# Kernel tuning notes

Hardware: AMD Instinct MI355X
Metric: run time of the kernel (lower is better)

The kernel has to match this reference:

```python
import jax, jax.numpy as jnp
import numpy as np

N_NODES = 2048
N_EDGES = 65536
IN_CH, HID_CH, OUT_CH = 512, 256, 128
NDIM = 5
THRESHOLD = 0.5


def _gcn(x, src, dst, ew, W, b):
    # GCNConv with self-loops (weight 1): D^{-1/2}(A+I)D^{-1/2} X W + b
    n = x.shape[0]
    deg = jnp.zeros((n,), x.dtype).at[dst].add(ew) + 1.0
    dinv = 1.0 / jnp.sqrt(deg)
    h = x @ W  # [N, out]
    coef = ew * dinv[src] * dinv[dst]  # [E]
    agg = jnp.zeros_like(h).at[dst].add(h[src] * coef[:, None])
    return agg + h / deg[:, None] + b


def _class_flags(feat, thr):
    # cosine similarity -> unnormalized Laplacian -> eigengap-based class ids
    xn = feat / (jnp.linalg.norm(feat, axis=1, keepdims=True) + 1e-8)
    S = xn @ xn.T  # [N, N]
    L = jnp.diag(jnp.sum(S, axis=1)) - S
    vals = jnp.linalg.eigvalsh(jax.lax.stop_gradient(L))  # ascending (class ids are non-diff)
    gaps = jnp.diff(vals)
    return jnp.concatenate([jnp.zeros((1,), jnp.int32),
                            jnp.cumsum((gaps > thr).astype(jnp.int32))])


def _class_avg(flags, feat):
    # per-class mean features, gathered back to each node
    n = feat.shape[0]
    sums = jax.ops.segment_sum(feat, flags, num_segments=n)
    cnts = jax.ops.segment_sum(jnp.ones((n,), feat.dtype), flags, num_segments=n)
    avg = sums / jnp.maximum(cnts, 1.0)[:, None]
    return avg[flags]


def _block(prev_gcn, skip, srcs, dsts, ews, convW, convb, linW, linb, k,
           changeW=None, changeb=None):
    gcn_out, outs = [], []
    for i in range(NDIM):
        g = _gcn(prev_gcn[i], srcs[i], dsts[i], ews[i], convW[i], convb[i])
        flags = _class_flags(g, THRESHOLD)
        lin = _class_avg(flags, g) @ linW + linb
        fir = skip[i] @ changeW + changeb if changeW is not None else skip[i]
        fea = fir + k * lin  # add_class_avg_to_node_features
        outs.append(jax.nn.relu(fir + fea))
        gcn_out.append(g)
    return gcn_out, outs


def _forward(dims, edge_indices, edge_weights, convWs, convbs, linWs, linbs,
             change1_W, change1_b, change2_W, change2_b, dimension_weights, k_save):
    srcs = [edge_indices[i, 0] for i in range(NDIM)]
    dsts = [edge_indices[i, 1] for i in range(NDIM)]
    ews = [edge_weights[i] for i in range(NDIM)]
    w = dimension_weights / jnp.sum(dimension_weights)
    g, out = _block(dims, dims, srcs, dsts, ews, convWs[0], convbs[0], linWs[0], linbs[0], k_save, change1_W, change1_b)
    g, out = _block(g, out, srcs, dsts, ews, convWs[1], convbs[1], linWs[1], linbs[1], k_save, change2_W, change2_b)
    for layer in range(2, 6):
        g, out = _block(g, out, srcs, dsts, ews, convWs[layer], convbs[layer], linWs[layer], linbs[layer], k_save)
    # dimension-weighted fusion of final per-dimension outputs
    return sum(w[i] * out[i] for i in range(NDIM))


def setup_inputs() -> dict:
    key = jax.random.key(0)
    ks = iter(jax.random.split(key, 80))
    def nrm(shape, s=0.05):
        return (jax.random.normal(next(ks), shape, jnp.float32) * s)
    inp = {}
    for i in range(NDIM):
        inp[f"dim{i+1}"] = jax.random.normal(next(ks), (N_NODES, IN_CH), jnp.float32)
    inp["edge_indices"] = jax.random.randint(next(ks), (NDIM, 2, N_EDGES), 0, N_NODES, jnp.int32)
    inp["edge_weights"] = jax.random.uniform(next(ks), (NDIM, N_EDGES), jnp.float32)
    inp["non_zero"] = N_NODES
    conv_shapes = [(IN_CH, HID_CH), (HID_CH, OUT_CH)] + [(OUT_CH, OUT_CH)] * 4
    for l, (ci, co) in enumerate(conv_shapes, start=1):
        inp[f"convW{l}"] = nrm((NDIM, ci, co))
        inp[f"convb{l}"] = nrm((NDIM, co))
    lin_shapes = [HID_CH, OUT_CH, OUT_CH, OUT_CH, OUT_CH, OUT_CH]
    names = ["preLin1", "preLin2", "preLin3", "behLin1", "behLin2", "behLin3"]
    for nm, c in zip(names, lin_shapes):
        inp[f"{nm}_W"] = nrm((c, c))
        inp[f"{nm}_b"] = nrm((c,))
    inp["change1_W"] = nrm((IN_CH, HID_CH)); inp["change1_b"] = nrm((HID_CH,))
    inp["change2_W"] = nrm((HID_CH, OUT_CH)); inp["change2_b"] = nrm((OUT_CH,))
    inp["dimension_weights"] = jnp.ones((NDIM,), jnp.float32)
    inp["k_save"] = jnp.float32(0.5)
    return inp


def reference(dim1, dim2, dim3, dim4, dim5, edge_indices, edge_weights, non_zero,
              convW1, convb1, convW2, convb2, convW3, convb3, convW4, convb4,
              convW5, convb5, convW6, convb6,
              preLin1_W, preLin1_b, preLin2_W, preLin2_b, preLin3_W, preLin3_b,
              behLin1_W, behLin1_b, behLin2_W, behLin2_b, behLin3_W, behLin3_b,
              change1_W, change1_b, change2_W, change2_b, dimension_weights, k_save):
    dims = [dim1, dim2, dim3, dim4, dim5]
    convWs = [convW1, convW2, convW3, convW4, convW5, convW6]
    convbs = [convb1, convb2, convb3, convb4, convb5, convb6]
    linWs = [preLin1_W, preLin2_W, preLin3_W, behLin1_W, behLin2_W, behLin3_W]
    linbs = [preLin1_b, preLin2_b, preLin3_b, behLin1_b, behLin2_b, behLin3_b]
    return _forward(dims, edge_indices, edge_weights, convWs, convbs, linWs, linbs,
                    change1_W, change1_b, change2_W, change2_b, dimension_weights, k_save)
```

## Files before the change

### kernel.cpp

```cpp
#include <hip/hip_runtime.h>
#include <math.h>
#include <stdint.h>

#define NN 2048
#define NE 65536
#define ND 5
#define DMX 256
#define MAXB1 2048
#define SUBD 8
#define NBF (MAXB1*SUBD+1)
#define NFMAX 1536
#define MAXRUN 1536
#define NPB 4
#define COARSE_H 1.76f
#define NUDGE 2e-3f
#define THRG 0.5f

typedef float f32x16 __attribute__((ext_vector_type(16)));
typedef float f32x8 __attribute__((ext_vector_type(8)));
typedef short s16x8 __attribute__((ext_vector_type(8)));
typedef unsigned short u16x8 __attribute__((ext_vector_type(8)));

__device__ __forceinline__ float wredSum(float v){
#pragma unroll
  for (int o=32;o>0;o>>=1) v += __shfl_down(v,o,64);
  return v;
}
__device__ __forceinline__ float wredMin(float v){
#pragma unroll
  for (int o=32;o>0;o>>=1) v = fminf(v,__shfl_down(v,o,64));
  return v;
}
__device__ __forceinline__ float wredMax(float v){
#pragma unroll
  for (int o=32;o>0;o>>=1) v = fmaxf(v,__shfl_down(v,o,64));
  return v;
}
__device__ __forceinline__ uint32_t encF(float f){
  uint32_t u = __float_as_uint(f);
  return (u & 0x80000000u) ? ~u : (u | 0x80000000u);
}
__device__ __forceinline__ float decF(uint32_t u){
  return (u & 0x80000000u) ? __uint_as_float(u ^ 0x80000000u) : __uint_as_float(~u);
}
__device__ __forceinline__ uint16_t bf16hi(float f){
  return (uint16_t)(__float_as_uint(f)>>16);
}

template<int BLK>
__device__ float bredSum(float v, float* red){
  v = wredSum(v);
  const int w = threadIdx.x >> 6;
  if ((threadIdx.x & 63) == 0) red[w] = v;
  __syncthreads();
  if (threadIdx.x == 0){
    float s = 0.f;
#pragma unroll
    for (int i=0;i<BLK/64;i++) s += red[i];
    red[0] = s;
  }
  __syncthreads();
  float r = red[0];
  __syncthreads();
  return r;
}

__global__ void k_prep(const float* __restrict__ xn, uint16_t* __restrict__ xph,
                       uint16_t* __restrict__ xpl, float* __restrict__ xpf, int co){
  const int dim = blockIdx.y;
  const int c2 = blockIdx.x;
  const int col = threadIdx.x;
  const float* x = xn + (size_t)dim*NN*co;
  const int kb = c2*8;
  u16x8 h8, l8;
  f32x8 f8;
#pragma unroll
  for (int j=0;j<8;j++){
    const float x0 = x[(size_t)(kb+j)*co + col];
    const uint16_t h = bf16hi(x0);
    h8[j] = h;
    l8[j] = bf16hi(x0 - __uint_as_float((uint32_t)h<<16));
    f8[j] = x0;
  }
  const size_t o = ((size_t)dim*(NN/8) + c2)*co + col;
  reinterpret_cast<u16x8*>(xph)[o] = h8;
  reinterpret_cast<u16x8*>(xpl)[o] = l8;
  reinterpret_cast<f32x8*>(xpf)[o] = f8;
}

template<int D, int BLK>
__device__ int evalNu(const uint16_t* __restrict__ xph, const uint16_t* __restrict__ xpl,
                      const float* __restrict__ xpf,
                      const float* __restrict__ a,
                      float t0, float dlt,
                      float* M, float* Pt, float* red, float* wrow,
                      float* scal, float* tOut)
{
  const int tid = threadIdx.x;
  float* fsc = scal + 16;

  float md = 1e30f;
  for (int i=tid;i<NN;i+=BLK) md = fminf(md, fabsf(a[i]-t0));
  md = wredMin(md);
  if ((tid & 63) == 0) red[tid>>6] = md;
  __syncthreads();
  if (tid == 0){
    float m2 = 1e30f;
    for (int i=0;i<BLK/64;i++) m2 = fminf(m2, red[i]);
    scal[1] = (m2 < 1e-3f) ? (t0 + dlt) : t0;
  }
  __syncthreads();
  const float t = scal[1];
  __syncthreads();

  float c = 0.f;
  for (int i=tid;i<NN;i+=BLK) c += (a[i] < t) ? 1.f : 0.f;
  float cnt = bredSum<BLK>(c, red);

  constexpr int BG  = D/64;
  constexpr int NBL = BG*(BG+1)/2;
  constexpr int SXT = 24;
  static_assert(BLK == NBL*64, "one wave per tile block");
  static_assert(2*D*SXT*2 <= (D*(D+1)/2)*4, "WX overlay fits in M");

  uint16_t* WXh = reinterpret_cast<uint16_t*>(M);
  uint16_t* WXl = WXh + D*SXT;
  const f32x8* XPF = reinterpret_cast<const f32x8*>(xpf);

  const int wv_ = tid >> 6, lane = tid & 63;
  int bi = 0, bj = 0;
  { int rem = wv_; while (rem >= BG - bi){ rem -= BG - bi; bi++; } bj = bi + rem; }
  const int colA = bi*64 + (lane & 31);
  const int colB = bj*64 + (lane & 31);
  const int kgo  = (lane >> 5) * 8;

  f32x16 acc0, acc1, acc2, acc3;
#pragma unroll
  for (int e=0;e<16;e++){ acc0[e]=0.f; acc1[e]=0.f; acc2[e]=0.f; acc3[e]=0.f; }

  if (tid < 16){
    float den = a[tid] - t;
    if (fabsf(den) < 1e-5f) den = (den < 0.f) ? -1e-5f : 1e-5f;
    wrow[tid] = 1.0f/den;
  }

  for (int k0=0; k0<NN; k0+=16){
    __syncthreads();
    const float* wcur = wrow + ((k0>>4)&1)*16;
    for (int it = tid; it < 2*D; it += BLK){
      const int kg  = it / D;
      const int col = it - kg*D;
      const f32x8 xv = XPF[(size_t)((k0>>3)+kg)*D + col];
      const float4 w0 = *reinterpret_cast<const float4*>(&wcur[kg*8]);
      const float4 w1 = *reinterpret_cast<const float4*>(&wcur[kg*8+4]);
      const float wv[8] = {w0.x,w0.y,w0.z,w0.w,w1.x,w1.y,w1.z,w1.w};
      u16x8 sph, spl;
#pragma unroll
      for (int j=0;j<8;j++){
        const float p0 = wv[j]*xv[j];
        const uint16_t hp = bf16hi(p0);
        sph[j] = hp;
        spl[j] = bf16hi(p0 - __uint_as_float((uint32_t)hp<<16));
      }
      const int base = col*SXT + kg*8;
      *reinterpret_cast<u16x8*>(WXh + base) = sph;
      *reinterpret_cast<u16x8*>(WXl + base) = spl;
    }
    if (tid < 16 && k0+16 < NN){
      float den = a[k0+16+tid] - t;
      if (fabsf(den) < 1e-5f) den = (den < 0.f) ? -1e-5f : 1e-5f;
      wrow[((((k0>>4)+1)&1)<<4) + tid] = 1.0f/den;
    }
    __syncthreads();
    const s16x8 ah0 = *reinterpret_cast<const s16x8*>(WXh + colA*SXT + kgo);
    const s16x8 ah1 = *reinterpret_cast<const s16x8*>(WXh + (colA+32)*SXT + kgo);
    const s16x8 al0 = *reinterpret_cast<const s16x8*>(WXl + colA*SXT + kgo);
    const s16x8 al1 = *reinterpret_cast<const s16x8*>(WXl + (colA+32)*SXT + kgo);
    const size_t cgB = (size_t)((k0>>3) + (lane>>5))*D;
    const s16x8 bh0 = *reinterpret_cast<const s16x8*>(xph + (cgB + colB)*8);
    const s16x8 bh1 = *reinterpret_cast<const s16x8*>(xph + (cgB + colB+32)*8);
    const s16x8 bl0 = *reinterpret_cast<const s16x8*>(xpl + (cgB + colB)*8);
    const s16x8 bl1 = *reinterpret_cast<const s16x8*>(xpl + (cgB + colB+32)*8);
    acc0 = __builtin_amdgcn_mfma_f32_32x32x16_bf16(ah0, bh0, acc0, 0,0,0);
    acc1 = __builtin_amdgcn_mfma_f32_32x32x16_bf16(ah0, bh1, acc1, 0,0,0);
    acc2 = __builtin_amdgcn_mfma_f32_32x32x16_bf16(ah1, bh0, acc2, 0,0,0);
    acc3 = __builtin_amdgcn_mfma_f32_32x32x16_bf16(ah1, bh1, acc3, 0,0,0);
    acc0 = __builtin_amdgcn_mfma_f32_32x32x16_bf16(ah0, bl0, acc0, 0,0,0);
    acc1 = __builtin_amdgcn_mfma_f32_32x32x16_bf16(ah0, bl1, acc1, 0,0,0);
    acc2 = __builtin_amdgcn_mfma_f32_32x32x16_bf16(ah1, bl0, acc2, 0,0,0);
    acc3 = __builtin_amdgcn_mfma_f32_32x32x16_bf16(ah1, bl1, acc3, 0,0,0);
    acc0 = __builtin_amdgcn_mfma_f32_32x32x16_bf16(al0, bh0, acc0, 0,0,0);
    acc1 = __builtin_amdgcn_mfma_f32_32x32x16_bf16(al0, bh1, acc1, 0,0,0);
    acc2 = __builtin_amdgcn_mfma_f32_32x32x16_bf16(al1, bh0, acc2, 0,0,0);
    acc3 = __builtin_amdgcn_mfma_f32_32x32x16_bf16(al1, bh1, acc3, 0,0,0);
  }
  __syncthreads();

  {
    const int rbase = 4*(lane>>5);
#pragma unroll
    for (int q=0;q<4;q++){
      const f32x16 A = (q==0)?acc0:((q==1)?acc1:((q==2)?acc2:acc3));
      const int ta = 2*bi + (q>>1), tb = 2*bj + (q&1);
      const int bb = tb*32 + (lane & 31);
#pragma unroll
      for (int r=0;r<16;r++){
        const int aa = ta*32 + (r&3) + 8*(r>>2) + rbase;
        if (aa <= bb)
          M[aa*D - (aa*(aa-1))/2 + (bb-aa)] = ((aa==bb)?1.f:0.f) - A[r];
      }
    }
  }

  constexpr int PS = 12;
  int neg = 0;
  for (int k0=0; k0<D; k0+=8){
    const int k1 = k0+8;
    __syncthreads();
    if (tid < 64){
      if (tid == 0){
        float B[8][8];
#pragma unroll
        for (int q=0;q<8;q++){
#pragma unroll
          for (int p=0;p<=q;p++){
            const int g = k0+p;
            B[p][q] = M[g*D - (g*(g-1))/2 + (k0+q-g)];
          }
        }
        float inv8[8];
#pragma unroll
        for (int q=0;q<8;q++){
          float d = B[q][q];
          if (d < 0.f) neg++;
          if (fabsf(d) < 1e-8f) d = (d<0.f)?-1e-8f:1e-8f;
          const float inv = 1.0f/d;
          inv8[q] = inv;
#pragma unroll
          for (int i=q+1;i<8;i++){
            const float f = B[q][i]*inv;
#pragma unroll
            for (int j=i;j<8;j++) B[i][j] = fmaf(-f, B[q][j], B[i][j]);
          }
        }
#pragma unroll
        for (int q=0;q<8;q++){
          fsc[36+q] = inv8[q];
#pragma unroll
          for (int p=0;p<=q;p++) fsc[(q*(q+1))/2 + p] = B[p][q];
        }
      }
      __asm__ __volatile__("s_waitcnt lgkmcnt(0)" ::: "memory");
      float c8[36], iv8[8];
#pragma unroll
      for (int k=0;k<36;k++) c8[k] = fsc[k];
#pragma unroll
      for (int k=0;k<8;k++) iv8[k] = fsc[36+k];
      for (int j = k1 + tid; j < D; j += 64){
        float rv[8], pt[8];
#pragma unroll
        for (int q=0;q<8;q++){
          const int g = k0+q;
          rv[q] = M[g*D - (g*(g-1))/2 + (j-g)];
        }
#pragma unroll
        for (int q=0;q<8;q++){
          float v = rv[q];
#pragma unroll
          for (int p=0;p<q;p++) v = fmaf(-c8[(q*(q+1))/2 + p], pt[p], v);
          pt[q] = v * iv8[q];
          const int g = k0+q;
          M[g*D - (g*(g-1))/2 + (j-g)] = v;
          Pt[j*PS + q] = pt[q];
        }
      }
    }
    __syncthreads();
    if (k1 < D){
      constexpr int G = BLK/4;
      const int grp = tid / G, sub = tid % G;
      for (int i0=k1; i0<D; i0+=4){
        const int i = i0 + grp;
        float cq[8];
#pragma unroll
        for (int q=0;q<8;q++){
          const int g = k0+q;
          cq[q] = M[g*D - (g*(g-1))/2 + (i-g)];
        }
        const int offi = i*D - (i*(i-1))/2;
        for (int j=i+sub; j<D; j+=G){
          const float4 p0 = *reinterpret_cast<const float4*>(&Pt[j*PS + 0]);
          const float4 p1 = *reinterpret_cast<const float4*>(&Pt[j*PS + 4]);
          float v = M[offi + (j-i)];
          v = fmaf(-cq[0],p0.x,v); v = fmaf(-cq[1],p0.y,v);
          v = fmaf(-cq[2],p0.z,v); v = fmaf(-cq[3],p0.w,v);
          v = fmaf(-cq[4],p1.x,v); v = fmaf(-cq[5],p1.y,v);
          v = fmaf(-cq[6],p1.z,v); v = fmaf(-cq[7],p1.w,v);
          M[offi + (j-i)] = v;
        }
      }
    }
  }
  if (tid == 0) ((int*)scal)[5] = neg;
  __syncthreads();
  const int negAll = ((int*)scal)[5];
  __syncthreads();

  *tOut = t;
  return negAll + (int)(cnt + 0.5f);
}

#define SMEM_D(D) (((D)*((D)+1)/2 + 12*(D) + 112)*4)

template<int D, int BLK, int WPE>
__global__ __launch_bounds__(BLK,WPE) void k_eval(const uint16_t* __restrict__ xph,
    const uint16_t* __restrict__ xpl, const float* __restrict__ xpf,
    const float* __restrict__ ab, const float* __restrict__ ctrlF,
    const int* __restrict__ ctrlI, int* __restrict__ nu1, float* __restrict__ tus1)
{
  const int dim = blockIdx.y;
  const int b = blockIdx.x;
  if (b > ctrlI[dim*8+0]) return;
  extern __shared__ float smem[];
  constexpr int TRI = D*(D+1)/2;
  float* M = smem; float* Pt = M+TRI; float* red = Pt + 12*D;
  float* wrow = red+16; float* scal = wrow+32;
  const float lo = ctrlF[dim*8+0], h1 = ctrlF[dim*8+1];
  float tU;
  int v = evalNu<D,BLK>(xph + (size_t)dim*NN*D, xpl + (size_t)dim*NN*D,
                        xpf + (size_t)dim*NN*D,
                        ab + dim*NN, lo + h1*b, NUDGE,
                        M,Pt,red,wrow,scal,&tU);
  if (threadIdx.x == 0){ nu1[dim*(MAXB1+1)+b] = v; tus1[dim*(MAXB1+1)+b] = tU; }
}

template<int D, int BLK, int WPE>
__global__ __launch_bounds__(BLK,WPE) void k_evalF(const uint16_t* __restrict__ xph,
    const uint16_t* __restrict__ xpl, const float* __restrict__ xpf,
    const float* __restrict__ ab, const float* __restrict__ ctrlF,
    const int* __restrict__ ctrlI, const int* __restrict__ fineBins,
    int* __restrict__ nuF, float* __restrict__ tusF)
{
  const int dim = blockIdx.y;
  const int task = blockIdx.x / (SUBD-1);
  int cnt = ctrlI[dim*8+3]; if (cnt > NFMAX) cnt = NFMAX;
  if (task >= cnt) return;
  const int s = blockIdx.x % (SUBD-1) + 1;
  const int bin = fineBins[dim*NFMAX + task];
  extern __shared__ float smem[];
  constexpr int TRI = D*(D+1)/2;
  float* M = smem; float* Pt = M+TRI; float* red = Pt + 12*D;
  float* wrow = red+16; float* scal = wrow+32;
  const float lo = ctrlF[dim*8+0], hf = ctrlF[dim*8+1]*(1.0f/SUBD);
  const int f = bin*SUBD + s;
  float tU;
  int v = evalNu<D,BLK>(xph + (size_t)dim*NN*D, xpl + (size_t)dim*NN*D,
                        xpf + (size_t)dim*NN*D,
                        ab + dim*NN, lo + hf*f, NUDGE,
                        M,Pt,red,wrow,scal,&tU);
  if (threadIdx.x == 0){ nuF[(size_t)dim*NBF+f] = v; tusF[(size_t)dim*NBF+f] = tU; }
}

template<int D, int BLK, int WPE>
__global__ __launch_bounds__(BLK,WPE) void k_probe(const uint16_t* __restrict__ xph,
    const uint16_t* __restrict__ xpl, const float* __restrict__ xpf,
    const float* __restrict__ ab, const int* __restrict__ ctrlI,
    const int* __restrict__ runP, const float* __restrict__ runB,
    int* __restrict__ nuP, float* __restrict__ tP)
{
  const int dim = blockIdx.y;
  const int r = blockIdx.x >> 3;
  int nr = ctrlI[dim*8+1]; if (nr > MAXRUN) nr = MAXRUN;
  if (r >= nr) return;
  const int side = (blockIdx.x >> 2) & 1;
  const int i = blockIdx.x & 3;
  extern __shared__ float smem[];
  constexpr int TRI = D*(D+1)/2;
  float* M = smem; float* Pt = M+TRI; float* red = Pt + 12*D;
  float* wrow = red+16; float* scal = wrow+32;
  const float* rb = runB + (size_t)(dim*MAXRUN + r)*4;
  const float lo = rb[side*2+0], hi = rb[side*2+1];
  const float t0 = lo + (hi - lo)*(float)(i+1)*(1.0f/(NPB+1));
  const float dlt = fminf(NUDGE, (hi-lo)*0.08f);
  float tU;
  int v = evalNu<D,BLK>(xph + (size_t)dim*NN*D, xpl + (size_t)dim*NN*D,
                        xpf + (size_t)dim*NN*D,
                        ab + dim*NN, t0, dlt,
                        M,Pt,red,wrow,scal,&tU);
  if (threadIdx.x == 0){
    const size_t o = (((size_t)dim*MAXRUN + r)*2 + side)*NPB + i;
    nuP[o] = v; tP[o] = tU;
  }
}

__global__ void k_decide(const int* __restrict__ ctrlI, const int* __restrict__ runP,
                         const float* __restrict__ runB, const int* __restrict__ nuP,
                         const float* __restrict__ tP, int* __restrict__ bnd){
  const int dim = blockIdx.x;
  int nr = ctrlI[dim*8+1]; if (nr > MAXRUN) nr = MAXRUN;
  for (int r = threadIdx.x; r < nr; r += blockDim.x){
    const int p = runP[dim*MAXRUN + r];
    const float* rb = runB + (size_t)(dim*MAXRUN + r)*4;
    float lam[2];
    for (int side=0; side<2; side++){
      const int rank = p + side;
      const size_t o = (((size_t)dim*MAXRUN + r)*2 + side)*NPB;
      float prev = rb[side*2+0];
      bool found = false; float l = 0.f;
      for (int i=0;i<NPB;i++){
        const float ti = tP[o+i];
        if (nuP[o+i] >= rank){ l = 0.5f*(prev + ti); found = true; break; }
        prev = ti;
      }
      if (!found) l = 0.5f*(prev + rb[side*2+1]);
      lam[side] = l;
    }
    if (lam[1] - lam[0] > THRG) bnd[dim*NN + p - 1] = 1;
  }
}

__global__ void k_sel(const int* __restrict__ nu1, int* ctrlI,
                      int* __restrict__ binSel, int* __restrict__ fineBins){
  const int dim = blockIdx.y;
  const int j = blockIdx.x*256 + threadIdx.x;
  const int nb1 = ctrlI[dim*8+0];
  if (j >= nb1) return;
  const int* nv = nu1 + dim*(MAXB1+1);
  if (nv[j+1] != nv[j]){
    const int slot = atomicAdd(&ctrlI[dim*8+3], 1);
    if (slot < NFMAX){ binSel[dim*MAXB1+j] = slot; fineBins[dim*NFMAX+slot] = j; }
    else binSel[dim*MAXB1+j] = -2;
  } else binSel[dim*MAXB1+j] = -1;
}

__global__ void k_fill(const int* __restrict__ nu1, const float* __restrict__ tus1,
                       const int* __restrict__ binSel, const float* __restrict__ ctrlF,
                       const int* __restrict__ ctrlI,
                       int* __restrict__ nuF, float* __restrict__ tusF){
  const int dim = blockIdx.y;
  const int f = blockIdx.x*256 + threadIdx.x;
  const int nb1 = ctrlI[dim*8+0];
  if (f > nb1*SUBD) return;
  const int j = f / SUBD, s = f % SUBD;
  const float lo = ctrlF[dim*8+0], hf = ctrlF[dim*8+1]*(1.0f/SUBD);
  int v; float tv;
  if (s == 0){ v = nu1[dim*(MAXB1+1)+j]; tv = tus1[dim*(MAXB1+1)+j]; }
  else {
    const int sel = binSel[dim*MAXB1+j];
    tv = lo + hf*f;
    if (sel == -2) v = 0x40000000 + f;
    else v = nu1[dim*(MAXB1+1)+j];
  }
  nuF[(size_t)dim*NBF+f] = v;
  tusF[(size_t)dim*NBF+f] = tv;
}

__global__ void k_runs(const int* __restrict__ nuF, const float* __restrict__ tusF,
                       int* ctrlI, int* __restrict__ runP, float* __restrict__ runB,
                       int* __restrict__ bnd){
  const int dim = blockIdx.y;
  const int b1 = blockIdx.x*256 + threadIdx.x;
  const int nbt = ctrlI[dim*8+0]*SUBD;
  if (b1 >= nbt) return;
  const int* nv = nuF + (size_t)dim*NBF;
  const float* tu = tusF + (size_t)dim*NBF;
  if (nv[b1+1] != nv[b1]) return;
  if (b1 > 0 && nv[b1-1] == nv[b1]) return;
  const int p = nv[b1];
  if (p < 1 || p > NN-1 || b1 < 1) return;
  const float tb1 = tu[b1];
  int j2 = b1;
  while (j2+1 < nbt && nv[j2+2] == nv[j2+1]){
    j2++;
    if (tu[j2+1] - tb1 > THRG){ bnd[dim*NN + p-1] = 1; return; }
  }
  if (j2 > nbt-2) return;
  const float gmin = tu[j2+1] - tb1;
  const float gmax = tu[j2+2] - tu[b1-1];
  if (gmin > THRG){ bnd[dim*NN + p-1] = 1; return; }
  if (gmax > THRG){
    const int slot = atomicAdd(&ctrlI[dim*8+1], 1);
    if (slot < MAXRUN){
      runP[dim*MAXRUN + slot] = p;
      float* rb = runB + (size_t)(dim*MAXRUN + slot)*4;
      rb[0]=tu[b1-1]; rb[1]=tu[b1]; rb[2]=tu[j2+1]; rb[3]=tu[j2+2];
    }
  }
}

__global__ void k_pw_init(float* __restrict__ vG, float* __restrict__ scACC){
  const int dim = blockIdx.x, tid = threadIdx.x;
  float* v = vG + (size_t)dim*NN;
  for (int i=tid;i<NN;i+=1024){
    uint32_t hsh = (uint32_t)i*2654435761u;
    v[i] = 1.0f + 2e-4f*(float)(hsh>>20);
  }
  if (tid == 0){ scACC[0*ND*2 + dim*2 + 0] = 1.0f; scACC[0*ND*2 + dim*2 + 1] = 0.f; }
}

template<int D>
__global__ __launch_bounds__(D) void k_pw_z(const float* __restrict__ xnb,
    const float* __restrict__ vG, float* __restrict__ zpart,
    float* __restrict__ scACC, int parReset){
  const int dim = blockIdx.y, seg = blockIdx.x, c = threadIdx.x;
  const float* x = xnb + (size_t)dim*NN*D;
  const float* v = vG + (size_t)dim*NN;
  const int i0 = seg*(NN/16);
  float acc = 0.f;
  for (int r=0;r<NN/16;r++){
    const int i = i0 + r;
    acc = fmaf(x[(size_t)i*D + c], v[i], acc);
  }
  zpart[((size_t)dim*16 + seg)*DMX + c] = acc;
  if (seg == 0 && c < 2) scACC[parReset*ND*2 + dim*2 + c] = 0.f;
}

template<int D>
__global__ __launch_bounds__(256) void k_pw_y(const float* __restrict__ xnb,
    const float* __restrict__ ab, const uint32_t* __restrict__ ctrlU,
    const float* __restrict__ zpart, float* __restrict__ vG,
    float* __restrict__ scACC, int parPrev, int parCur){
  constexpr int VEC = D/64;
  const int dim = blockIdx.y, seg = blockIdx.x, tid = threadIdx.x;
  const int w = tid >> 6, lane = tid & 63;
  const float* x = xnb + (size_t)dim*NN*D;
  const float* a = ab + dim*NN;
  float* v = vG + (size_t)dim*NN;
  __shared__ float zs[DMX];
  __shared__ float redn[4], redr[4];
  if (tid < D){
    float s = 0.f;
#pragma unroll
    for (int k=0;k<16;k++) s += zpart[((size_t)dim*16 + k)*DMX + tid];
    zs[tid] = s;
  }
  __syncthreads();
  const float amax = decF(ctrlU[dim*8+1]);
  const float invPrev = rsqrtf(fmaxf(scACC[parPrev*ND*2 + dim*2 + 0], 1e-30f));
  float zr[VEC];
#pragma unroll
  for (int k=0;k<VEC;k++) zr[k] = zs[lane*VEC + k];
  float n2 = 0.f, ray = 0.f;
  for (int r=0;r<32;r++){
    const int i = seg*(NN/16) + w*32 + r;
    const float* xr = x + (size_t)i*D + lane*VEC;
    float dot = 0.f;
#pragma unroll
    for (int k=0;k<VEC;k++) dot = fmaf(xr[k], zr[k], dot);
#pragma unroll
    for (int o=32;o>0;o>>=1) dot += __shfl_xor(dot,o,64);
    if (lane == 0){
      const float vr = v[i];
      const float y = invPrev * fmaf(amax - a[i], vr, dot);
      n2 = fmaf(y,y,n2); ray = fmaf(vr*invPrev, y, ray);
      v[i] = y;
    }
  }
  if (lane == 0){ redn[w] = n2; redr[w] = ray; }
  __syncthreads();
  if (tid == 0){
    float sn = redn[0]+redn[1]+redn[2]+redn[3];
    float sr = redr[0]+redr[1]+redr[2]+redr[3];
    atomicAdd(&scACC[parCur*ND*2 + dim*2 + 0], sn);
    atomicAdd(&scACC[parCur*ND*2 + dim*2 + 1], sr);
  }
}

__global__ void k_pw_fin(const float* __restrict__ scACC, float* __restrict__ thB,
                         int slot){
  if (threadIdx.x < ND) thB[threadIdx.x] = scACC[slot*ND*2 + threadIdx.x*2 + 1];
}

__global__ void k_init(float* deg, int* cur){
  const int dim = blockIdx.x;
  for (int i=threadIdx.x;i<NN;i+=blockDim.x){ deg[dim*NN+i] = 1.0f; cur[dim*NN+i] = 0; }
}
__global__ void k_count(const int* __restrict__ eidx, const float* __restrict__ ew,
                        float* deg, int* cur){
  const int idx = blockIdx.x*256 + threadIdx.x;
  if (idx >= ND*NE) return;
  const int dim = idx / NE, e = idx % NE;
  const int dst = eidx[(size_t)dim*2*NE + NE + e];
  atomicAdd(&cur[dim*NN + dst], 1);
  atomicAdd(&deg[dim*NN + dst], ew[(size_t)dim*NE + e]);
}
__global__ void k_prefix(int* cur, int* base){
  const int dim = blockIdx.x;
  if (threadIdx.x) return;
  int* b = base + dim*(NN+1);
  int* cc = cur + dim*NN;
  int run = 0; b[0] = 0;
  for (int i=0;i<NN;i++){ int cnt = cc[i]; cc[i] = run; b[i+1] = run + cnt; run += cnt; }
}
__global__ void k_fill_csr(const int* __restrict__ eidx, const float* __restrict__ ew,
                       const float* __restrict__ deg, int* cur, int* psrc, float* coef){
  const int idx = blockIdx.x*256 + threadIdx.x;
  if (idx >= ND*NE) return;
  const int dim = idx / NE, e = idx % NE;
  const int src = eidx[(size_t)dim*2*NE + e];
  const int dst = eidx[(size_t)dim*2*NE + NE + e];
  const int slot = atomicAdd(&cur[dim*NN + dst], 1);
  psrc[(size_t)dim*NE + slot] = src;
  const float ds = deg[dim*NN + src], dd = deg[dim*NN + dst];
  coef[(size_t)dim*NE + slot] = ew[(size_t)dim*NE + e] * (1.0f/sqrtf(ds)) * (1.0f/sqrtf(dd));
}
__global__ void k_selfw(const float* deg, float* sw){
  const int idx = blockIdx.x*256 + threadIdx.x;
  if (idx < ND*NN) sw[idx] = 1.0f/deg[idx];
}

__global__ __launch_bounds__(256) void k_gemm(const float* __restrict__ A, long long aStr,
    const float* __restrict__ W, long long wStr,
    const float* __restrict__ bias, long long bStr,
    float* __restrict__ C, long long cStr, int M, int K, int P)
{
  const int dim = blockIdx.z;
  A += (size_t)dim*aStr; W += (size_t)dim*wStr; C += (size_t)dim*cStr;
  if (bias) bias += (size_t)dim*bStr;
  __shared__ float As[64][17];
  __shared__ float Bs[16][68];
  const int tid = threadIdx.x;
  const int tx = tid % 16, ty = tid / 16;
  const int m0 = blockIdx.y*64, p0 = blockIdx.x*64;
  float acc[4][4] = {};
  for (int k0=0;k0<K;k0+=16){
    __syncthreads();
    { int r = tid/4, c4 = (tid%4)*4;
      float4 v = *reinterpret_cast<const float4*>(A + (size_t)(m0+r)*K + k0 + c4);
      As[r][c4]=v.x; As[r][c4+1]=v.y; As[r][c4+2]=v.z; As[r][c4+3]=v.w; }
    { int r = tid/16, c4 = (tid%16)*4;
      float4 v = *reinterpret_cast<const float4*>(W + (size_t)(k0+r)*P + p0 + c4);
      Bs[r][c4]=v.x; Bs[r][c4+1]=v.y; Bs[r][c4+2]=v.z; Bs[r][c4+3]=v.w; }
    __syncthreads();
#pragma unroll
    for (int kk=0;kk<16;kk++){
      float a0=As[ty*4+0][kk], a1=As[ty*4+1][kk], a2=As[ty*4+2][kk], a3=As[ty*4+3][kk];
      float b0=Bs[kk][tx*4+0], b1=Bs[kk][tx*4+1], b2=Bs[kk][tx*4+2], b3=Bs[kk][tx*4+3];
      acc[0][0]=fmaf(a0,b0,acc[0][0]); acc[0][1]=fmaf(a0,b1,acc[0][1]);
      acc[0][2]=fmaf(a0,b2,acc[0][2]); acc[0][3]=fmaf(a0,b3,acc[0][3]);
      acc[1][0]=fmaf(a1,b0,acc[1][0]); acc[1][1]=fmaf(a1,b1,acc[1][1]);
      acc[1][2]=fmaf(a1,b2,acc[1][2]); acc[1][3]=fmaf(a1,b3,acc[1][3]);
      acc[2][0]=fmaf(a2,b0,acc[2][0]); acc[2][1]=fmaf(a2,b1,acc[2][1]);
      acc[2][2]=fmaf(a2,b2,acc[2][2]); acc[2][3]=fmaf(a2,b3,acc[2][3]);
      acc[3][0]=fmaf(a3,b0,acc[3][0]); acc[3][1]=fmaf(a3,b1,acc[3][1]);
      acc[3][2]=fmaf(a3,b2,acc[3][2]); acc[3][3]=fmaf(a3,b3,acc[3][3]);
    }
  }
  for (int i=0;i<4;i++){
    for (int j=0;j<4;j++){
      const int pp = p0 + tx*4 + j;
      float v = acc[i][j];
      if (bias) v += bias[pp];
      C[(size_t)(m0+ty*4+i)*P + pp] = v;
    }
  }
}

__global__ void k_agg(const float* __restrict__ h, float* __restrict__ g,
                      const float* __restrict__ convb, const int* __restrict__ base,
                      const int* __restrict__ psrc, const float* __restrict__ coef,
                      const float* __restrict__ selfw, int co)
{
  const int i = blockIdx.x, dim = blockIdx.y, c = threadIdx.x;
  const float* hD = h + (size_t)dim*NN*co;
  const int s = base[dim*(NN+1)+i], e = base[dim*(NN+1)+i+1];
  const int* ps = psrc + (size_t)dim*NE;
  const float* cf = coef + (size_t)dim*NE;
  float acc = 0.f;
  for (int q=s;q<e;q++) acc += cf[q]*hD[(size_t)ps[q]*co + c];
  g[((size_t)dim*NN+i)*co + c] = acc + hD[(size_t)i*co + c]*selfw[dim*NN+i] + convb[dim*co + c];
}

__global__ void k_rownorm(const float* __restrict__ g, float* __restrict__ xn, int co){
  const int i = blockIdx.x, dim = blockIdx.y;
  const float* gr = g + ((size_t)dim*NN+i)*co;
  float* xr = xn + ((size_t)dim*NN+i)*co;
  float p = 0.f;
  for (int c=threadIdx.x;c<co;c+=256){ float v = gr[c]; p += v*v; }
  __shared__ float red[4];
  p = wredSum(p);
  if ((threadIdx.x&63)==0) red[threadIdx.x>>6] = p;
  __syncthreads();
  if (threadIdx.x==0) red[0] = red[0]+red[1]+red[2]+red[3];
  __syncthreads();
  const float inv = 1.0f/(sqrtf(red[0]) + 1e-8f);
  for (int c=threadIdx.x;c<co;c+=256) xr[c] = gr[c]*inv;
}

__global__ void k_colsum(const float* __restrict__ xn, float* __restrict__ sb, int co){
  const int lane = threadIdx.x & 63;
  const int seg  = threadIdx.x >> 6;
  const int c = blockIdx.x*64 + lane;
  const int dim = blockIdx.y;
  const float* x = xn + (size_t)dim*NN*co;
  float s = 0.f;
  for (int i=seg*(NN/4); i<(seg+1)*(NN/4); i++) s += x[(size_t)i*co + c];
  __shared__ float part[4][64];
  part[seg][lane] = s;
  __syncthreads();
  if (threadIdx.x < 64)
    sb[dim*DMX + c] = part[0][lane]+part[1][lane]+part[2][lane]+part[3][lane];
}

__global__ __launch_bounds__(512) void k_adot(const float* __restrict__ xn,
                       const float* __restrict__ sb,
                       float* __restrict__ ab, uint32_t* ctrlU, int co){
  const int dim = blockIdx.y;
  const int w = threadIdx.x >> 6, lane = threadIdx.x & 63;
  const int i = blockIdx.x*8 + w;
  const float* x = xn + ((size_t)dim*NN + i)*co;
  const float* s = sb + dim*DMX;
  float p = 0.f;
  for (int c=lane;c<co;c+=64) p = fmaf(x[c], s[c], p);
  p = wredSum(p);
  __shared__ uint32_t rmn[8], rmx[8];
  if (lane==0){
    ab[dim*NN+i] = p;
    const uint32_t e = encF(p);
    rmn[w] = e; rmx[w] = e;
  }
  __syncthreads();
  if (threadIdx.x==0){
    uint32_t mn = rmn[0], mx = rmx[0];
#pragma unroll
    for (int k=1;k<8;k++){
      mn = (rmn[k] < mn) ? rmn[k] : mn;
      mx = (rmx[k] > mx) ? rmx[k] : mx;
    }
    atomicMin(&ctrlU[dim*8+0], mn);
    atomicMax(&ctrlU[dim*8+1], mx);
  }
}

__global__ __launch_bounds__(256) void k_gramC(const float* __restrict__ xn,
                                               float* __restrict__ Cb, int co){
  const int dim = blockIdx.y;
  const int nbx = co/32;
  const int bx = blockIdx.x % nbx, by = blockIdx.x / nbx;
  const float* x = xn + (size_t)dim*NN*co;
  float* C = Cb + (size_t)dim*co*co;
  __shared__ float Xa[64][33];
  __shared__ float Xb[64][33];
  const int tid = threadIdx.x;
  const int ty = tid/16, tx = tid%16;
  float a00=0,a01=0,a10=0,a11=0;
  for (int i0=0;i0<NN;i0+=64){
    __syncthreads();
    for (int l=tid;l<512;l+=256){
      const int r = l/8, c4 = (l%8)*4;
      float4 va = *reinterpret_cast<const float4*>(x + (size_t)(i0+r)*co + by*32 + c4);
      Xa[r][c4]=va.x; Xa[r][c4+1]=va.y; Xa[r][c4+2]=va.z; Xa[r][c4+3]=va.w;
      float4 vb = *reinterpret_cast<const float4*>(x + (size_t)(i0+r)*co + bx*32 + c4);
      Xb[r][c4]=vb.x; Xb[r][c4+1]=vb.y; Xb[r][c4+2]=vb.z; Xb[r][c4+3]=vb.w;
    }
    __syncthreads();
#pragma unroll 8
    for (int r=0;r<64;r++){
      const float u0=Xa[r][ty*2], u1=Xa[r][ty*2+1], w0=Xb[r][tx*2], w1=Xb[r][tx*2+1];
      a00=fmaf(u0,w0,a00); a01=fmaf(u0,w1,a01); a10=fmaf(u1,w0,a10); a11=fmaf(u1,w1,a11);
    }
  }
  const int ca = by*32 + ty*2, cb = bx*32 + tx*2;
  C[(size_t)(ca+0)*co + cb+0]=a00; C[(size_t)(ca+0)*co + cb+1]=a01;
  C[(size_t)(ca+1)*co + cb+0]=a10; C[(size_t)(ca+1)*co + cb+1]=a11;
}

__global__ void k_layerinit(int* bnd, uint32_t* ctrlU, int* ctrlI){
  const int dim = blockIdx.x;
  for (int i=threadIdx.x;i<NN;i+=blockDim.x) bnd[dim*NN+i] = 0;
  if (threadIdx.x==0){
    ctrlU[dim*8+0] = 0xFFFFFFFFu;
    ctrlU[dim*8+1] = 0u;
    ctrlI[dim*8+1] = 0;
    ctrlI[dim*8+3] = 0;
  }
}

__global__ __launch_bounds__(256) void k_bounds(const float* __restrict__ Cb,
                         const uint32_t* ctrlU, const float* __restrict__ thB,
                         float* ctrlF, int* ctrlI, int co){
  const int dim = blockIdx.x, tid = threadIdx.x;
  const float* C = Cb + (size_t)dim*co*co;
  __shared__ float red[4];
  float rs = 0.f;
  if (tid < co){
    const float* row = C + (size_t)tid*co;
    for (int b=0;b<co;b++) rs += fabsf(row[b]);
  }
  float mx = wredMax(rs);
  if ((tid&63)==0) red[tid>>6] = mx;
  __syncthreads();
  if (tid==0){
    const float gersh = fmaxf(fmaxf(red[0],red[1]), fmaxf(red[2],red[3]));
    const float amin = decF(ctrlU[dim*8+0]);
    const float amax = decF(ctrlU[dim*8+1]);
    const float th = thB[dim];
    const float loG = amin - gersh;
    const float loP = amax - th - (0.02f*fabsf(th) + 0.5f);
    const float lo = fmaxf(loG, loP) - 0.05f;
    const float hi = amax + 0.1f;
    int nb = (int)ceilf((hi - lo)/COARSE_H);
    if (nb > MAXB1) nb = MAXB1;
    if (nb < 8) nb = 8;
    ctrlF[dim*8+0] = lo;
    ctrlF[dim*8+1] = (hi - lo)/nb;
    ctrlI[dim*8+0] = nb;
  }
}

__global__ void k_flags(const int* __restrict__ bnd, int* flags, int* cstart, int* ctrlI){
  const int dim = blockIdx.x;
  if (threadIdx.x) return;
  const int* b = bnd + dim*NN;
  int* f = flags + dim*NN;
  int* cs = cstart + dim*(NN+1);
  int cur = 0; f[0] = 0; cs[0] = 0;
  for (int i=1;i<NN;i++){
    cur += b[i-1];
    f[i] = cur;
    if (b[i-1]) cs[cur] = i;
  }
  ctrlI[dim*8+2] = cur+1;
  cs[cur+1] = NN;
}

__global__ void k_cavg(const float* __restrict__ g, const int* __restrict__ cstart,
                       const int* __restrict__ ctrlI, float* __restrict__ cavg, int co){
  const int dim = blockIdx.y;
  const int nc = ctrlI[dim*8+2];
  const float* gD = g + (size_t)dim*NN*co;
  const int cc = threadIdx.x;
  for (int c = blockIdx.x; c < nc; c += gridDim.x){
    const int s = cstart[dim*(NN+1)+c], e = cstart[dim*(NN+1)+c+1];
    const float inv = 1.0f/(float)(e - s);
    if (cc < co){
      float acc = 0.f;
      for (int i=s;i<e;i++) acc += gD[(size_t)i*co + cc];
      cavg[((size_t)dim*NN + c)*co + cc] = acc*inv;
    }
  }
}

__global__ void k_clin(const float* __restrict__ cavg, const float* __restrict__ linW,
                       const float* __restrict__ linb, float* __restrict__ clin,
                       const int* __restrict__ ctrlI, int co){
  const int dim = blockIdx.y;
  const int nc = ctrlI[dim*8+2];
  __shared__ float row[DMX];
  const int tid = threadIdx.x;
  for (int c = blockIdx.x; c < nc; c += gridDim.x){
    const float* av = cavg + ((size_t)dim*NN + c)*co;
    __syncthreads();
    if (tid < co) row[tid] = av[tid];
    __syncthreads();
    if (tid < co){
      float s = linb[tid];
      for (int k=0;k<co;k++) s = fmaf(row[k], linW[(size_t)k*co + tid], s);
      clin[((size_t)dim*NN + c)*co + tid] = s;
    }
  }
}

__global__ void k_out(const float* __restrict__ fir, const float* __restrict__ clin,
                      const int* __restrict__ flags, const float* __restrict__ ksv,
                      float* __restrict__ out, int co){
  const int i = blockIdx.x, dim = blockIdx.y, c = threadIdx.x;
  const float kv = ksv[0];
  const int cls = flags[dim*NN+i];
  const float fv = fir[((size_t)dim*NN+i)*co + c];
  const float lv = clin[((size_t)dim*NN+cls)*co + c];
  const float o = 2.f*fv + kv*lv;
  out[((size_t)dim*NN+i)*co + c] = (o > 0.f) ? o : 0.f;
}

__global__ void k_final(const float* __restrict__ outL, const float* __restrict__ dimw,
                        float* __restrict__ o){
  const int i = blockIdx.x, c = threadIdx.x;
  float w[ND]; float ws = 0.f;
#pragma unroll
  for (int d=0;d<ND;d++){ w[d] = dimw[d]; ws += w[d]; }
  float v = 0.f;
#pragma unroll
  for (int d=0;d<ND;d++) v += (w[d]/ws) * outL[((size_t)d*NN + i)*128 + c];
  o[(size_t)i*128 + c] = v;
}

extern "C" void kernel_launch(void* const* d_in, const int* in_sizes, int n_in,
                              void* d_out, int out_size, void* d_ws, size_t ws_size,
                              hipStream_t stream)
{
  const float* dims_in[ND];
  for (int d=0;d<ND;d++) dims_in[d] = (const float*)d_in[d];
  const int*   eidx = (const int*)d_in[5];
  const float* ew   = (const float*)d_in[6];
  const float* convW[6]; const float* convb[6];
  for (int l=0;l<6;l++){ convW[l] = (const float*)d_in[8+2*l]; convb[l] = (const float*)d_in[9+2*l]; }
  const float* linW[6]; const float* linb[6];
  for (int l=0;l<6;l++){ linW[l] = (const float*)d_in[20+2*l]; linb[l] = (const float*)d_in[21+2*l]; }
  const float* ch1W = (const float*)d_in[32]; const float* ch1b = (const float*)d_in[33];
  const float* ch2W = (const float*)d_in[34]; const float* ch2b = (const float*)d_in[35];
  const float* dimw = (const float*)d_in[36]; const float* ksv = (const float*)d_in[37];

  char* p = (char*)d_ws;
  auto take = [&](size_t bytes)->char*{
    char* r = p; p += (bytes + 255) & ~(size_t)255; return r;
  };
  int*   csr_base = (int*)  take((size_t)ND*(NN+1)*4);
  int*   csr_cur  = (int*)  take((size_t)ND*NN*4);
  int*   csr_psrc = (int*)  take((size_t)ND*NE*4);
  float* csr_coef = (float*)take((size_t)ND*NE*4);
  float* deg      = (float*)take((size_t)ND*NN*4);
  float* selfw    = (float*)take((size_t)ND*NN*4);
  float* gA   = (float*)take((size_t)ND*NN*DMX*4);
  float* gB   = (float*)take((size_t)ND*NN*DMX*4);
  float* outA = (float*)take((size_t)ND*NN*DMX*4);
  float* outB = (float*)take((size_t)ND*NN*DMX*4);
  float* hbuf = (float*)take((size_t)ND*NN*DMX*4);
  float* xnbuf= (float*)take((size_t)ND*NN*DMX*4);
  float* cavg = (float*)take((size_t)ND*NN*DMX*4);
  uint16_t* xph = (uint16_t*)take((size_t)ND*NN*DMX*2);
  uint16_t* xpl = (uint16_t*)take((size_t)ND*NN*DMX*2);
  float* xpf  = (float*)take((size_t)ND*NN*DMX*4);
  float* abuf = (float*)take((size_t)ND*NN*4);
  float* sbuf = (float*)take((size_t)ND*DMX*4);
  float* Cbuf = (float*)take((size_t)ND*DMX*DMX*4);
  float* vpow = (float*)take((size_t)ND*NN*4);
  float* zpartG=(float*)take((size_t)ND*16*DMX*4);
  float* scACC =(float*)take((size_t)2*ND*2*4);
  int*   nu1  = (int*)  take((size_t)ND*(MAXB1+1)*4);
  float* tus1 = (float*)take((size_t)ND*(MAXB1+1)*4);
  int*   nuF  = (int*)  take((size_t)ND*NBF*4);
  float* tusF = (float*)take((size_t)ND*NBF*4);
  int*   binSel=(int*)  take((size_t)ND*MAXB1*4);
  int*   fineBins=(int*)take((size_t)ND*NFMAX*4);
  int*   runP = (int*)  take((size_t)ND*MAXRUN*4);
  float* runB = (float*)take((size_t)ND*MAXRUN*4*4);
  int*   nuP  = (int*)  take((size_t)ND*MAXRUN*2*NPB*4);
  float* tP   = (float*)take((size_t)ND*MAXRUN*2*NPB*4);
  int*   bnd  = (int*)  take((size_t)ND*NN*4);
  int*   flagsA=(int*)  take((size_t)ND*NN*4);
  int*   cstart=(int*)  take((size_t)ND*(NN+1)*4);
  float* ctrlF= (float*)take((size_t)ND*8*4);
  uint32_t* ctrlU = (uint32_t*)take((size_t)ND*8*4);
  int*   ctrlI= (int*)  take((size_t)ND*8*4);
  float* thB  = (float*)take((size_t)ND*4);
  (void)ws_size; (void)in_sizes; (void)n_in; (void)out_size;

  {
    void (*pe)(const uint16_t*,const uint16_t*,const float*,const float*,const float*,const int*,int*,float*) = k_eval<256,640,1>;
    hipFuncSetAttribute((const void*)pe, hipFuncAttributeMaxDynamicSharedMemorySize, SMEM_D(256));
    void (*pf)(const uint16_t*,const uint16_t*,const float*,const float*,const float*,const int*,const int*,int*,float*) = k_evalF<256,640,1>;
    hipFuncSetAttribute((const void*)pf, hipFuncAttributeMaxDynamicSharedMemorySize, SMEM_D(256));
    void (*pp)(const uint16_t*,const uint16_t*,const float*,const float*,const int*,const int*,const float*,int*,float*) = k_probe<256,640,1>;
    hipFuncSetAttribute((const void*)pp, hipFuncAttributeMaxDynamicSharedMemorySize, SMEM_D(256));
  }

  k_init<<<ND, 256, 0, stream>>>(deg, csr_cur);
  k_count<<<(ND*NE+255)/256, 256, 0, stream>>>(eidx, ew, deg, csr_cur);
  k_prefix<<<ND, 64, 0, stream>>>(csr_cur, csr_base);
  k_fill_csr<<<(ND*NE+255)/256, 256, 0, stream>>>(eidx, ew, deg, csr_cur, csr_psrc, csr_coef);
  k_selfw<<<(ND*NN+255)/256, 256, 0, stream>>>(deg, selfw);

  float* gbufs[2] = {gA, gB};
  float* obufs[2] = {outA, outB};
  const float* gPrev = nullptr;
  const float* oPrev = nullptr;

  for (int l=0;l<6;l++){
    const int co = (l==0) ? 256 : 128;
    const int ci = (l==0) ? 512 : ((l==1) ? 256 : 128);
    float* gCur = gbufs[l&1];
    float* oCur = obufs[l&1];

    if (l==0){
      for (int d=0;d<ND;d++)
        k_gemm<<<dim3(256/64, NN/64, 1), 256, 0, stream>>>(
          dims_in[d], 0, convW[0] + (size_t)d*512*256, 0, nullptr, 0,
          hbuf + (size_t)d*NN*256, 0, NN, 512, 256);
    } else {
      k_gemm<<<dim3(co/64, NN/64, ND), 256, 0, stream>>>(
        gPrev, (long long)NN*ci, convW[l], (long long)ci*co, nullptr, 0,
        hbuf, (long long)NN*co, NN, ci, co);
    }

    k_layerinit<<<ND, 256, 0, stream>>>(bnd, ctrlU, ctrlI);
    k_agg<<<dim3(NN, ND), co, 0, stream>>>(hbuf, gCur, convb[l], csr_base, csr_psrc,
                                           csr_coef, selfw, co);
    k_rownorm<<<dim3(NN, ND), 256, 0, stream>>>(gCur, xnbuf, co);
    k_prep<<<dim3(NN/8, ND), co, 0, stream>>>(xnbuf, xph, xpl, xpf, co);
    k_colsum<<<dim3(co/64, ND), 256, 0, stream>>>(xnbuf, sbuf, co);
    k_adot<<<dim3(NN/8, ND), 512, 0, stream>>>(xnbuf, sbuf, abuf, ctrlU, co);
    k_gramC<<<dim3((co/32)*(co/32), ND), 256, 0, stream>>>(xnbuf, Cbuf, co);

    k_pw_init<<<ND, 1024, 0, stream>>>(vpow, scACC);
    if (l==0){
      for (int it=0; it<33; it++){
        const int sp = it & 1, sc = sp ^ 1;
        k_pw_z<256><<<dim3(16, ND), 256, 0, stream>>>(xnbuf, vpow, zpartG, scACC, sc);
        k_pw_y<256><<<dim3(16, ND), 256, 0, stream>>>(xnbuf, abuf, ctrlU, zpartG, vpow, scACC, sp, sc);
      }
    } else {
      for (int it=0; it<33; it++){
        const int sp = it & 1, sc = sp ^ 1;
        k_pw_z<128><<<dim3(16, ND), 128, 0, stream>>>(xnbuf, vpow, zpartG, scACC, sc);
        k_pw_y<128><<<dim3(16, ND), 256, 0, stream>>>(xnbuf, abuf, ctrlU, zpartG, vpow, scACC, sp, sc);
      }
    }
    k_pw_fin<<<1, 64, 0, stream>>>(scACC, thB, 1);

    k_bounds<<<ND, 256, 0, stream>>>(Cbuf, ctrlU, thB, ctrlF, ctrlI, co);

    if (l==0){
      k_eval<256,640,1><<<dim3(MAXB1+1, ND), 640, SMEM_D(256), stream>>>(xph, xpl, xpf, abuf, ctrlF, ctrlI, nu1, tus1);
      k_sel<<<dim3((MAXB1+255)/256, ND), 256, 0, stream>>>(nu1, ctrlI, binSel, fineBins);
      k_fill<<<dim3((NBF+255)/256, ND), 256, 0, stream>>>(nu1, tus1, binSel, ctrlF, ctrlI, nuF, tusF);
      k_evalF<256,640,1><<<dim3(NFMAX*(SUBD-1), ND), 640, SMEM_D(256), stream>>>(xph, xpl, xpf, abuf, ctrlF, ctrlI, fineBins, nuF, tusF);
      k_runs<<<dim3((NBF+255)/256, ND), 256, 0, stream>>>(nuF, tusF, ctrlI, runP, runB, bnd);
      k_probe<256,640,1><<<dim3(MAXRUN*2*NPB, ND), 640, SMEM_D(256), stream>>>(xph, xpl, xpf, abuf, ctrlI, runP, runB, nuP, tP);
      k_decide<<<ND, 256, 0, stream>>>(ctrlI, runP, runB, nuP, tP, bnd);
    } else {
      k_eval<128,192,4><<<dim3(MAXB1+1, ND), 192, SMEM_D(128), stream>>>(xph, xpl, xpf, abuf, ctrlF, ctrlI, nu1, tus1);
      k_sel<<<dim3((MAXB1+255)/256, ND), 256, 0, stream>>>(nu1, ctrlI, binSel, fineBins);
      k_fill<<<dim3((NBF+255)/256, ND), 256, 0, stream>>>(nu1, tus1, binSel, ctrlF, ctrlI, nuF, tusF);
      k_evalF<128,192,4><<<dim3(NFMAX*(SUBD-1), ND), 192, SMEM_D(128), stream>>>(xph, xpl, xpf, abuf, ctrlF, ctrlI, fineBins, nuF, tusF);
      k_runs<<<dim3((NBF+255)/256, ND), 256, 0, stream>>>(nuF, tusF, ctrlI, runP, runB, bnd);
      k_probe<128,192,4><<<dim3(MAXRUN*2*NPB, ND), 192, SMEM_D(128), stream>>>(xph, xpl, xpf, abuf, ctrlI, runP, runB, nuP, tP);
      k_decide<<<ND, 256, 0, stream>>>(ctrlI, runP, runB, nuP, tP, bnd);
    }

    k_flags<<<ND, 64, 0, stream>>>(bnd, flagsA, cstart, ctrlI);
    k_cavg<<<dim3(128, ND), 256, 0, stream>>>(gCur, cstart, ctrlI, cavg, co);
    k_clin<<<dim3(128, ND), 256, 0, stream>>>(cavg, linW[l], linb[l], xnbuf, ctrlI, co);

    const float* firPtr;
    if (l==0){
      for (int d=0;d<ND;d++)
        k_gemm<<<dim3(256/64, NN/64, 1), 256, 0, stream>>>(
          dims_in[d], 0, ch1W, 0, ch1b, 0, hbuf + (size_t)d*NN*256, 0, NN, 512, 256);
      firPtr = hbuf;
    } else if (l==1){
      k_gemm<<<dim3(128/64, NN/64, ND), 256, 0, stream>>>(
        oPrev, (long long)NN*256, ch2W, 0, ch2b, 0, hbuf, (long long)NN*128, NN, 256, 128);
      firPtr = hbuf;
    } else {
      firPtr = oPrev;
    }

    k_out<<<dim3(NN, ND), co, 0, stream>>>(firPtr, xnbuf, flagsA, ksv, oCur, co);

    gPrev = gCur; oPrev = oCur;
  }

  k_final<<<NN, 128, 0, stream>>>(oPrev, dimw, (float*)d_out);
}
```

Before: 33.91 ms.

## Double-buffer WX staging to overlap LDS staging with MFMA accumulation

Splits the LDS-staged weighted matrix product loop into stage, weight-compute and MFMA steps. Two WX buffers in shared memory let the next chunk be staged while the MFMAs consume the current one, which removes one barrier per k-chunk. The cost is twice the LDS overlay inside M and a more intricate schedule that depends on the weight-row slot alternation being correct.

New measurement: 33.18 ms. 1.02x faster.

```diff
diff --git a/kernel.cpp b/kernel.cpp
--- a/kernel.cpp
+++ b/kernel.cpp
@@ -120,11 +120,14 @@
   constexpr int BG  = D/64;
   constexpr int NBL = BG*(BG+1)/2;
   constexpr int SXT = 24;
+  constexpr int NCH = NN/16;
   static_assert(BLK == NBL*64, "one wave per tile block");
-  static_assert(2*D*SXT*2 <= (D*(D+1)/2)*4, "WX overlay fits in M");
-
-  uint16_t* WXh = reinterpret_cast<uint16_t*>(M);
-  uint16_t* WXl = WXh + D*SXT;
+  static_assert(4*D*SXT*2 <= (D*(D+1)/2)*4, "WX dbuf overlay fits in M");
+
+  uint16_t* WX0h = reinterpret_cast<uint16_t*>(M);
+  uint16_t* WX0l = WX0h + D*SXT;
+  uint16_t* WX1h = WX0l + D*SXT;
+  uint16_t* WX1l = WX1h + D*SXT;
   const f32x8* XPF = reinterpret_cast<const f32x8*>(xpf);
 
   const int wv_ = tid >> 6, lane = tid & 63;
@@ -138,45 +141,40 @@
 #pragma unroll
   for (int e=0;e<16;e++){ acc0[e]=0.f; acc1[e]=0.f; acc2[e]=0.f; acc3[e]=0.f; }
 
-  if (tid < 16){
-    float den = a[tid] - t;
-    if (fabsf(den) < 1e-5f) den = (den < 0.f) ? -1e-5f : 1e-5f;
-    wrow[tid] = 1.0f/den;
-  }
-
-  for (int k0=0; k0<NN; k0+=16){
-    __syncthreads();
-    const float* wcur = wrow + ((k0>>4)&1)*16;
+  auto WCOMP = [&](int ch, int slot){
+    if (tid < 16 && ch < NCH){
+      float den = a[16*ch + tid] - t;
+      if (fabsf(den) < 1e-5f) den = (den < 0.f) ? -1e-5f : 1e-5f;
+      wrow[slot*16 + tid] = 1.0f/den;
+    }
+  };
+  auto STAGE = [&](int ch, uint16_t* Wh, uint16_t* Wl, const float* wc){
     for (int it = tid; it < 2*D; it += BLK){
       const int kg  = it / D;
       const int col = it - kg*D;
-      const f32x8 xv = XPF[(size_t)((k0>>3)+kg)*D + col];
-      const float4 w0 = *reinterpret_cast<const float4*>(&wcur[kg*8]);
-      const float4 w1 = *reinterpret_cast<const float4*>(&wcur[kg*8+4]);
-      const float wv[8] = {w0.x,w0.y,w0.z,w0.w,w1.x,w1.y,w1.z,w1.w};
+      const f32x8 xv = XPF[(size_t)(ch*2 + kg)*D + col];
+      const float4 w0 = *reinterpret_cast<const float4*>(&wc[kg*8]);
+      const float4 w1 = *reinterpret_cast<const float4*>(&wc[kg*8+4]);
+      const float wvv[8] = {w0.x,w0.y,w0.z,w0.w,w1.x,w1.y,w1.z,w1.w};
       u16x8 sph, spl;
 #pragma unroll
       for (int j=0;j<8;j++){
-        const float p0 = wv[j]*xv[j];
+        const float p0 = wvv[j]*xv[j];
         const uint16_t hp = bf16hi(p0);
         sph[j] = hp;
         spl[j] = bf16hi(p0 - __uint_as_float((uint32_t)hp<<16));
       }
       const int base = col*SXT + kg*8;
-      *reinterpret_cast<u16x8*>(WXh + base) = sph;
-      *reinterpret_cast<u16x8*>(WXl + base) = spl;
-    }
-    if (tid < 16 && k0+16 < NN){
-      float den = a[k0+16+tid] - t;
-      if (fabsf(den) < 1e-5f) den = (den < 0.f) ? -1e-5f : 1e-5f;
-      wrow[((((k0>>4)+1)&1)<<4) + tid] = 1.0f/den;
-    }
-    __syncthreads();
-    const s16x8 ah0 = *reinterpret_cast<const s16x8*>(WXh + colA*SXT + kgo);
-    const s16x8 ah1 = *reinterpret_cast<const s16x8*>(WXh + (colA+32)*SXT + kgo);
-    const s16x8 al0 = *reinterpret_cast<const s16x8*>(WXl + colA*SXT + kgo);
-    const s16x8 al1 = *reinterpret_cast<const s16x8*>(WXl + (colA+32)*SXT + kgo);
-    const size_t cgB = (size_t)((k0>>3) + (lane>>5))*D;
+      *reinterpret_cast<u16x8*>(Wh + base) = sph;
+      *reinterpret_cast<u16x8*>(Wl + base) = spl;
+    }
+  };
+  auto MSTEP = [&](int ch, const uint16_t* Wh, const uint16_t* Wl){
+    const s16x8 ah0 = *reinterpret_cast<const s16x8*>(Wh + colA*SXT + kgo);
+    const s16x8 ah1 = *reinterpret_cast<const s16x8*>(Wh + (colA+32)*SXT + kgo);
+    const s16x8 al0 = *reinterpret_cast<const s16x8*>(Wl + colA*SXT + kgo);
+    const s16x8 al1 = *reinterpret_cast<const s16x8*>(Wl + (colA+32)*SXT + kgo);
+    const size_t cgB = (size_t)(ch*2 + (lane>>5))*D;
     const s16x8 bh0 = *reinterpret_cast<const s16x8*>(xph + (cgB + colB)*8);
     const s16x8 bh1 = *reinterpret_cast<const s16x8*>(xph + (cgB + colB+32)*8);
     const s16x8 bl0 = *reinterpret_cast<const s16x8*>(xpl + (cgB + colB)*8);
@@ -193,8 +191,23 @@
     acc1 = __builtin_amdgcn_mfma_f32_32x32x16_bf16(al0, bh1, acc1, 0,0,0);
     acc2 = __builtin_amdgcn_mfma_f32_32x32x16_bf16(al1, bh0, acc2, 0,0,0);
     acc3 = __builtin_amdgcn_mfma_f32_32x32x16_bf16(al1, bh1, acc3, 0,0,0);
-  }
-  __syncthreads();
+  };
+
+  WCOMP(0, 0);
+  __syncthreads();
+  STAGE(0, WX0h, WX0l, wrow + 0);
+  WCOMP(1, 1);
+  __syncthreads();
+  for (int ch = 0; ch < NCH; ch += 2){
+    STAGE(ch+1, WX1h, WX1l, wrow + 16);
+    WCOMP(ch+2, 0);
+    MSTEP(ch, WX0h, WX0l);
+    __syncthreads();
+    if (ch+2 < NCH) STAGE(ch+2, WX0h, WX0l, wrow + 0);
+    WCOMP(ch+3, 1);
+    MSTEP(ch+1, WX1h, WX1l);
+    __syncthreads();
+  }
 
   {
     const int rbase = 4*(lane>>5);
```
